# Kernel tuning notes

Measured on AMD Instinct MI355X. Metric: run time of the kernel, lower is better.

The kernel has to match this reference:

```python
import jax, jax.numpy as jnp
import numpy as np

N_NODES = 50000
N_EDGES = 1_600_000
N_GRAPHS = 64
EMB = 1280
GCN_DIMS = [128, 256, 256]
FC_DIMS = [1024, 128]
EPS = 1e-5  # BatchNorm eps (torch default)


def setup_inputs() -> dict:
    key = jax.random.key(0)
    ks = jax.random.split(key, 16)
    inp = {}
    inp["x"] = jax.random.normal(ks[0], (N_NODES, EMB), jnp.float32)
    inp["edge_index"] = jax.random.randint(ks[1], (2, N_EDGES), 0, N_NODES)
    inp["batch"] = jnp.sort(jax.random.randint(ks[2], (N_NODES,), 0, N_GRAPHS))
    dims = [EMB] + GCN_DIMS
    for i in range(3):
        inp[f"Wg{i}"] = jax.random.normal(ks[3 + i], (dims[i], dims[i + 1]), jnp.float32) * (1.0 / np.sqrt(dims[i]))
        inp[f"bg{i}"] = jnp.zeros((dims[i + 1],), jnp.float32)
        inp[f"gamma{i}"] = jnp.ones((dims[i + 1],), jnp.float32)
        inp[f"beta{i}"] = jnp.zeros((dims[i + 1],), jnp.float32)
    fdims = [GCN_DIMS[-1]] + FC_DIMS
    for i in range(2):
        inp[f"Wf{i}"] = jax.random.normal(ks[10 + i], (fdims[i], fdims[i + 1]), jnp.float32) * (1.0 / np.sqrt(fdims[i]))
        inp[f"bf{i}"] = jnp.zeros((fdims[i + 1],), jnp.float32)
    return inp


def _batchnorm(h, gamma, beta):
    # training-mode BN over node dim, biased variance (torch normalization)
    m = h.mean(axis=0)
    v = h.var(axis=0)
    return gamma * (h - m) * jax.lax.rsqrt(v + EPS) + beta


def reference(x, edge_index, batch,
              Wg0, bg0, gamma0, beta0,
              Wg1, bg1, gamma1, beta1,
              Wg2, bg2, gamma2, beta2,
              Wf0, bf0, Wf1, bf1):
    # --- GCN symmetric normalization with self-loops (PyG GCNConv default) ---
    loop = jnp.arange(N_NODES)
    src = jnp.concatenate([edge_index[0], loop])  # message sources
    dst = jnp.concatenate([edge_index[1], loop])  # aggregation targets
    deg = jax.ops.segment_sum(jnp.ones(src.shape[0], jnp.float32), dst, num_segments=N_NODES)
    dinv = jnp.where(deg > 0, jax.lax.rsqrt(jnp.maximum(deg, 1.0)), 0.0)
    norm = dinv[src] * dinv[dst]  # [E + N]

    def gcn_conv(h, W, b):
        h = h @ W                               # [N, d_out] transform first (PyG order)
        msg = h[src] * norm[:, None]            # gather + scale
        return jax.ops.segment_sum(msg, dst, num_segments=N_NODES) + b

    h = x
    for W, b, g, bt in ((Wg0, bg0, gamma0, beta0),
                        (Wg1, bg1, gamma1, beta1),
                        (Wg2, bg2, gamma2, beta2)):
        h = gcn_conv(h, W, b)
        h = _batchnorm(h, g, bt)
        h = jax.nn.relu(h)
        # dropout is identity in eval mode

    # --- global mean pool over graphs ---
    counts = jax.ops.segment_sum(jnp.ones(N_NODES, jnp.float32), batch, num_segments=N_GRAPHS)
    sums = jax.ops.segment_sum(h, batch, num_segments=N_GRAPHS)
    g = sums / jnp.maximum(counts, 1.0)[:, None]  # [B, 256]

    # --- FC head ---
    g = jax.nn.relu(g @ Wf0 + bf0)
    out = g @ Wf1 + bf1                           # [B, 128]
    return out
```

## Files before the change

kernel.cpp:

```cpp
#include <hip/hip_runtime.h>
#include <hip/hip_bf16.h>

#define N_NODES 50000
#define N_EDGES 1600000
#define N_GRAPHS 64

typedef _Float16 f16;
typedef _Float16 f16x8 __attribute__((ext_vector_type(8)));
typedef _Float16 f16x4 __attribute__((ext_vector_type(4)));
typedef _Float16 f16x2 __attribute__((ext_vector_type(2)));
typedef float f32x4 __attribute__((ext_vector_type(4)));

template <int V> struct VecT;
template <> struct VecT<2> { using type = f16x2; };
template <> struct VecT<4> { using type = f16x4; };

__global__ void init_deg(int* deg) {
    int i = blockIdx.x * blockDim.x + threadIdx.x;
    if (i < N_NODES) deg[i] = 1;
}

__global__ void deg_count(const int* __restrict__ dst, int* __restrict__ deg) {
    int e = blockIdx.x * blockDim.x + threadIdx.x;
    if (e < N_EDGES) atomicAdd(&deg[dst[e]], 1);
}

__global__ void make_dinv(const int* __restrict__ deg, float* __restrict__ dinv) {
    int i = blockIdx.x * blockDim.x + threadIdx.x;
    if (i < N_NODES) dinv[i] = rsqrtf((float)deg[i]);
}

__global__ void scan_deg(const int* __restrict__ deg, int* __restrict__ rowstart,
                         int* __restrict__ pos) {
    __shared__ int wsum[16];
    __shared__ int carry_s;
    const int t = threadIdx.x;
    const int lane = t & 63;
    const int w = t >> 6;
    if (t == 0) carry_s = 0;
    __syncthreads();
    for (int base = 0; base < N_NODES; base += 1024) {
        int i = base + t;
        int v = (i < N_NODES) ? (deg[i] - 1) : 0;
        int s = v;
#pragma unroll
        for (int off = 1; off < 64; off <<= 1) {
            int n = __shfl_up(s, off, 64);
            if (lane >= off) s += n;
        }
        if (lane == 63) wsum[w] = s;
        __syncthreads();
        if (w == 0) {
            int ws = (lane < 16) ? wsum[lane] : 0;
#pragma unroll
            for (int off = 1; off < 16; off <<= 1) {
                int n = __shfl_up(ws, off, 64);
                if (lane >= off) ws += n;
            }
            if (lane < 16) wsum[lane] = ws;
        }
        __syncthreads();
        int waveoff = (w == 0) ? 0 : wsum[w - 1];
        int carry = carry_s;
        int excl = carry + waveoff + s - v;
        if (i < N_NODES) {
            rowstart[i] = excl;
            pos[i] = excl;
        }
        __syncthreads();
        if (t == 0) carry_s = carry + wsum[15];
        __syncthreads();
    }
    if (t == 0) rowstart[N_NODES] = carry_s;
}

__global__ void csr_fill(const int* __restrict__ src, const int* __restrict__ dst,
                         const float* __restrict__ dinv, int* __restrict__ pos,
                         int2* __restrict__ csr) {
    int e = blockIdx.x * blockDim.x + threadIdx.x;
    if (e >= N_EDGES) return;
    int s = src[e], d = dst[e];
    int slot = atomicAdd(&pos[d], 1);
    csr[slot] = make_int2(s, __float_as_int(dinv[s] * dinv[d]));
}

__global__ void cast_w(const float* __restrict__ W, f16* __restrict__ Wt, int K, int N) {
    int i = blockIdx.x * blockDim.x + threadIdx.x;
    if (i >= K * N) return;
    int k = i % K, n = i / K;
    Wt[i] = (f16)W[(size_t)k * N + n];
}

__launch_bounds__(256)
__global__ void gemm_x_f16_sk(const float* __restrict__ A, const f16* __restrict__ Bt,
                              float* __restrict__ C0, float* __restrict__ C1,
                              float* __restrict__ C2, float* __restrict__ C3,
                              int M, int K) {
    const int gw = (int)((blockIdx.x * blockDim.x + threadIdx.x) >> 6);
    const int lane = threadIdx.x & 63;
    const int tile = gw >> 2, s = gw & 3;
    const int m0 = tile * 32;
    if (m0 >= M) return;
    float* __restrict__ C = (s == 0) ? C0 : (s == 1) ? C1 : (s == 2) ? C2 : C3;
    const int KC = K >> 2;
    const int kbeg = s * KC;
    const int r = lane & 15, q = lane >> 4;
    int row0 = m0 + r;       int row0c = row0 < M ? row0 : M - 1;
    int row1 = m0 + 16 + r;  int row1c = row1 < M ? row1 : M - 1;
    const float* a0 = A + (size_t)row0c * K + q * 8;
    const float* a1 = A + (size_t)row1c * K + q * 8;
    const f16* bp = Bt + (size_t)r * K + q * 8;

    f32x4 acc[2][8];
#pragma unroll
    for (int i = 0; i < 2; ++i)
#pragma unroll
        for (int j = 0; j < 8; ++j) acc[i][j] = (f32x4){0.f, 0.f, 0.f, 0.f};

    for (int k0 = kbeg; k0 < kbeg + KC; k0 += 32) {
        f16x8 af[2];
        {
            float4 u = *(const float4*)(a0 + k0);
            float4 v = *(const float4*)(a0 + k0 + 4);
            af[0] = (f16x8){(f16)u.x, (f16)u.y, (f16)u.z, (f16)u.w,
                            (f16)v.x, (f16)v.y, (f16)v.z, (f16)v.w};
            u = *(const float4*)(a1 + k0);
            v = *(const float4*)(a1 + k0 + 4);
            af[1] = (f16x8){(f16)u.x, (f16)u.y, (f16)u.z, (f16)u.w,
                            (f16)v.x, (f16)v.y, (f16)v.z, (f16)v.w};
        }
#pragma unroll
        for (int ni = 0; ni < 8; ++ni) {
            f16x8 bf = *(const f16x8*)(bp + (size_t)ni * 16 * K + k0);
            acc[0][ni] = __builtin_amdgcn_mfma_f32_16x16x32_f16(af[0], bf, acc[0][ni], 0, 0, 0);
            acc[1][ni] = __builtin_amdgcn_mfma_f32_16x16x32_f16(af[1], bf, acc[1][ni], 0, 0, 0);
        }
    }
#pragma unroll
    for (int mi = 0; mi < 2; ++mi)
#pragma unroll
        for (int j = 0; j < 4; ++j) {
            int row = m0 + mi * 16 + q * 4 + j;
            if (row < M) {
                float* cp = C + (size_t)row * 128 + r;
#pragma unroll
                for (int ni = 0; ni < 8; ++ni) cp[ni * 16] = acc[mi][ni][j];
            }
        }
}

__global__ void reduce_cast4(const float* __restrict__ c0, const float* __restrict__ c1,
                             const float* __restrict__ c2, const float* __restrict__ c3,
                             f16* __restrict__ o, int n4) {
    int i = blockIdx.x * blockDim.x + threadIdx.x;
    if (i >= n4) return;
    float4 a = ((const float4*)c0)[i];
    float4 b = ((const float4*)c1)[i];
    float4 c = ((const float4*)c2)[i];
    float4 d = ((const float4*)c3)[i];
    f16x4 r = {(f16)(a.x + b.x + c.x + d.x), (f16)(a.y + b.y + c.y + d.y),
               (f16)(a.z + b.z + c.z + d.z), (f16)(a.w + b.w + c.w + d.w)};
    ((f16x4*)o)[i] = r;
}

template <int K>
__launch_bounds__(256)
__global__ void gemm_h_f16(const f16* __restrict__ A16, const f16* __restrict__ Bt,
                           f16* __restrict__ C16, int M, int N) {
    const int wave = (int)((blockIdx.x * blockDim.x + threadIdx.x) >> 6);
    const int lane = threadIdx.x & 63;
    const int m0 = wave * 32;
    if (m0 >= M) return;
    const int col0 = blockIdx.y * 128;
    const int r = lane & 15, q = lane >> 4;
    int row0 = m0 + r;       int row0c = row0 < M ? row0 : M - 1;
    int row1 = m0 + 16 + r;  int row1c = row1 < M ? row1 : M - 1;
    const f16* a0 = A16 + (size_t)row0c * K + q * 8;
    const f16* a1 = A16 + (size_t)row1c * K + q * 8;
    const f16* bp = Bt + (size_t)(col0 + r) * K + q * 8;

    f32x4 acc[2][8];
#pragma unroll
    for (int i = 0; i < 2; ++i)
#pragma unroll
        for (int j = 0; j < 8; ++j) acc[i][j] = (f32x4){0.f, 0.f, 0.f, 0.f};

#pragma unroll
    for (int k0 = 0; k0 < K; k0 += 32) {
        f16x8 af0 = *(const f16x8*)(a0 + k0);
        f16x8 af1 = *(const f16x8*)(a1 + k0);
#pragma unroll
        for (int ni = 0; ni < 8; ++ni) {
            f16x8 bf = *(const f16x8*)(bp + (size_t)ni * 16 * K + k0);
            acc[0][ni] = __builtin_amdgcn_mfma_f32_16x16x32_f16(af0, bf, acc[0][ni], 0, 0, 0);
            acc[1][ni] = __builtin_amdgcn_mfma_f32_16x16x32_f16(af1, bf, acc[1][ni], 0, 0, 0);
        }
    }
#pragma unroll
    for (int mi = 0; mi < 2; ++mi)
#pragma unroll
        for (int j = 0; j < 4; ++j) {
            int row = m0 + mi * 16 + q * 4 + j;
            if (row < M) {
                f16* cp = C16 + (size_t)row * N + col0 + r;
#pragma unroll
                for (int ni = 0; ni < 8; ++ni) cp[ni * 16] = (f16)acc[mi][ni][j];
            }
        }
}

template <int D>
__launch_bounds__(256)
__global__ void aggregate(const f16* __restrict__ h, const int* __restrict__ rowstart,
                          const int2* __restrict__ csr, const float* __restrict__ dinv,
                          const float* __restrict__ bias, f16* __restrict__ out) {
    constexpr int V = D / 64;
    using vec = typename VecT<V>::type;
    int w = (int)((blockIdx.x * blockDim.x + threadIdx.x) >> 6);
    int lane = threadIdx.x & 63;
    if (w >= N_NODES) return;
    float acc[V];
    float di = dinv[w];
    vec self = *(const vec*)(h + (size_t)w * D + lane * V);
#pragma unroll
    for (int v = 0; v < V; ++v) acc[v] = (float)self[v] * (di * di);
    int e0 = rowstart[w], e1 = rowstart[w + 1];
    int j = e0;
    for (; j + 8 <= e1; j += 8) {
        int2 c[8];
        vec rr[8];
#pragma unroll
        for (int u = 0; u < 8; ++u) c[u] = csr[j + u];
#pragma unroll
        for (int u = 0; u < 8; ++u)
            rr[u] = *(const vec*)(h + (size_t)c[u].x * D + lane * V);
#pragma unroll
        for (int u = 0; u < 8; ++u) {
            float nm = __int_as_float(c[u].y);
#pragma unroll
            for (int v = 0; v < V; ++v) acc[v] += (float)rr[u][v] * nm;
        }
    }
    if (j + 4 <= e1) {
        int2 c0 = csr[j], c1 = csr[j + 1], c2 = csr[j + 2], c3 = csr[j + 3];
        vec r0 = *(const vec*)(h + (size_t)c0.x * D + lane * V);
        vec r1 = *(const vec*)(h + (size_t)c1.x * D + lane * V);
        vec r2 = *(const vec*)(h + (size_t)c2.x * D + lane * V);
        vec r3 = *(const vec*)(h + (size_t)c3.x * D + lane * V);
        float n0 = __int_as_float(c0.y), n1 = __int_as_float(c1.y);
        float n2 = __int_as_float(c2.y), n3 = __int_as_float(c3.y);
#pragma unroll
        for (int v = 0; v < V; ++v)
            acc[v] += (float)r0[v] * n0 + (float)r1[v] * n1 +
                      (float)r2[v] * n2 + (float)r3[v] * n3;
        j += 4;
    }
    for (; j < e1; ++j) {
        int2 c = csr[j];
        vec r = *(const vec*)(h + (size_t)c.x * D + lane * V);
        float nm = __int_as_float(c.y);
#pragma unroll
        for (int v = 0; v < V; ++v) acc[v] += (float)r[v] * nm;
    }
    vec o;
#pragma unroll
    for (int v = 0; v < V; ++v) o[v] = (f16)(acc[v] + bias[lane * V + v]);
    *(vec*)(out + (size_t)w * D + lane * V) = o;
}

template <int D>
__global__ void bn_stats(const f16* __restrict__ h, float* __restrict__ stat) {
    int f = threadIdx.x;
    int r0 = blockIdx.x * 128;
    int r1 = min(r0 + 128, N_NODES);
    float s = 0.f, s2 = 0.f;
    for (int r = r0; r < r1; ++r) {
        float v = (float)h[(size_t)r * D + f];
        s += v;
        s2 += v * v;
    }
    atomicAdd(&stat[f], s);
    atomicAdd(&stat[D + f], s2);
}

template <int D>
__global__ void bn_finalize(const float* __restrict__ stat, const float* __restrict__ gamma,
                            const float* __restrict__ beta, float* __restrict__ ss) {
    int f = threadIdx.x;
    float m = stat[f] * (1.0f / N_NODES);
    float var = stat[D + f] * (1.0f / N_NODES) - m * m;
    float sc = gamma[f] * rsqrtf(var + 1e-5f);
    ss[f] = sc;
    ss[D + f] = beta[f] - m * sc;
}

template <int D>
__global__ void bn_apply_relu(const f16* __restrict__ hin, const float* __restrict__ ss,
                              f16* __restrict__ hout) {
    int i = blockIdx.x * blockDim.x + threadIdx.x;
    if (i >= N_NODES * D / 8) return;
    int f0 = (i * 8) & (D - 1);
    f16x8 v = ((const f16x8*)hin)[i];
    f16x8 r;
#pragma unroll
    for (int j = 0; j < 8; ++j) {
        float val = (float)v[j] * ss[f0 + j] + ss[D + f0 + j];
        r[j] = (f16)(val > 0.f ? val : 0.f);
    }
    ((f16x8*)hout)[i] = r;
}

__global__ void count_batch_bs(const int* __restrict__ batch, int* __restrict__ cnt) {
    int g = threadIdx.x;
    if (g >= N_GRAPHS) return;
    int lo = 0, hi = N_NODES;
    while (lo < hi) { int mid = (lo + hi) >> 1; if (batch[mid] < g) lo = mid + 1; else hi = mid; }
    int b0 = lo;
    lo = 0; hi = N_NODES;
    while (lo < hi) { int mid = (lo + hi) >> 1; if (batch[mid] < g + 1) lo = mid + 1; else hi = mid; }
    cnt[g] = lo - b0;
}

__global__ void pool_seg(const f16* __restrict__ h, const int* __restrict__ batch,
                         float* __restrict__ psum) {
    int f = threadIdx.x;
    int r0 = blockIdx.x * 64;
    int r1 = min(r0 + 64, N_NODES);
    float acc = 0.f;
    int cur = batch[r0];
    for (int r = r0; r < r1; ++r) {
        int b = batch[r];
        if (b != cur) {
            atomicAdd(&psum[cur * 256 + f], acc);
            acc = 0.f;
            cur = b;
        }
        acc += (float)h[(size_t)r * 256 + f];
    }
    atomicAdd(&psum[cur * 256 + f], acc);
}

__global__ void pool_div(const float* __restrict__ psum, const int* __restrict__ cnt,
                         float* __restrict__ g) {
    int i = blockIdx.x * 256 + threadIdx.x;
    int b = i >> 8;
    float c = (float)max(cnt[b], 1);
    g[i] = psum[i] / c;
}

__global__ void fc_init(const float* __restrict__ b, float* __restrict__ Y, int rows, int N) {
    int i = blockIdx.x * blockDim.x + threadIdx.x;
    if (i < rows * N) Y[i] = b[i % N];
}

__global__ void fc_splitk(const float* __restrict__ X, const float* __restrict__ W,
                          float* __restrict__ Y, int K, int N, int KC) {
    int col = blockIdx.x * blockDim.x + threadIdx.x;
    int row = blockIdx.y;
    int k0 = blockIdx.z * KC;
    float acc = 0.f;
    const float* x = X + (size_t)row * K + k0;
    const float* w = W + (size_t)k0 * N + col;
#pragma unroll 8
    for (int k = 0; k < KC; ++k) acc += x[k] * w[(size_t)k * N];
    atomicAdd(&Y[(size_t)row * N + col], acc);
}

__global__ void relu_inplace(float* __restrict__ Y, int n) {
    int i = blockIdx.x * blockDim.x + threadIdx.x;
    if (i < n) Y[i] = Y[i] > 0.f ? Y[i] : 0.f;
}

extern "C" void kernel_launch(void* const* d_in, const int* in_sizes, int n_in,
                              void* d_out, int out_size, void* d_ws, size_t ws_size,
                              hipStream_t stream) {
    const float* x     = (const float*)d_in[0];
    const int*   ei    = (const int*)d_in[1];
    const int*   batch = (const int*)d_in[2];
    const float* Wg0 = (const float*)d_in[3],  *bg0 = (const float*)d_in[4];
    const float* gamma0 = (const float*)d_in[5], *beta0 = (const float*)d_in[6];
    const float* Wg1 = (const float*)d_in[7],  *bg1 = (const float*)d_in[8];
    const float* gamma1 = (const float*)d_in[9], *beta1 = (const float*)d_in[10];
    const float* Wg2 = (const float*)d_in[11], *bg2 = (const float*)d_in[12];
    const float* gamma2 = (const float*)d_in[13], *beta2 = (const float*)d_in[14];
    const float* Wf0 = (const float*)d_in[15], *bf0 = (const float*)d_in[16];
    const float* Wf1 = (const float*)d_in[17], *bf1 = (const float*)d_in[18];
    float* out = (float*)d_out;

    size_t off = 0;
    auto alloc = [&](size_t bytes) {
        void* p = (char*)d_ws + off;
        off += (bytes + 255) & ~(size_t)255;
        return p;
    };
    f16*   hA16     = (f16*)alloc((size_t)N_NODES * 256 * 2);
    float* cp32     = (float*)alloc((size_t)4 * N_NODES * 128 * 4);
    f16*   hBn16    = (f16*)cp32;
    f16*   h16      = (f16*)(cp32 + (size_t)N_NODES * 128);
    float* cp0      = cp32;
    float* cp1      = cp32 + (size_t)N_NODES * 128;
    float* cp2      = cp32 + (size_t)2 * N_NODES * 128;
    float* cp3      = cp32 + (size_t)3 * N_NODES * 128;
    int2*  csr      = (int2*)alloc((size_t)N_EDGES * 8);
    int*   deg      = (int*)alloc((size_t)N_NODES * 4);
    float* dinv     = (float*)alloc((size_t)N_NODES * 4);
    int*   rowstart = (int*)alloc((size_t)(N_NODES + 1) * 4);
    int*   pos      = (int*)alloc((size_t)N_NODES * 4);
    float* bnstat   = (float*)alloc(2 * 256 * 4);
    float* bnss     = (float*)alloc(2 * 256 * 4);
    float* psum     = (float*)alloc(64 * 256 * 4);
    int*   pcount   = (int*)alloc(64 * 4);
    float* gpool    = (float*)alloc(64 * 256 * 4);
    float* g1       = (float*)alloc(64 * 1024 * 4);
    f16*   W0t      = (f16*)alloc((size_t)1280 * 128 * 2);
    f16*   W1t      = (f16*)alloc((size_t)128 * 256 * 2);
    f16*   W2t      = (f16*)alloc((size_t)256 * 256 * 2);
    (void)ws_size;

    const int TPB = 256;
    const int nb_nodes = (N_NODES + TPB - 1) / TPB;
    const int nb_edges = (N_EDGES + TPB - 1) / TPB;

    init_deg<<<nb_nodes, TPB, 0, stream>>>(deg);
    deg_count<<<nb_edges, TPB, 0, stream>>>(ei + N_EDGES, deg);
    make_dinv<<<nb_nodes, TPB, 0, stream>>>(deg, dinv);
    scan_deg<<<1, 1024, 0, stream>>>(deg, rowstart, pos);
    csr_fill<<<nb_edges, TPB, 0, stream>>>(ei, ei + N_EDGES, dinv, pos, csr);
    cast_w<<<(1280 * 128 + 255) / 256, 256, 0, stream>>>(Wg0, W0t, 1280, 128);
    cast_w<<<(128 * 256 + 255) / 256, 256, 0, stream>>>(Wg1, W1t, 128, 256);
    cast_w<<<(256 * 256 + 255) / 256, 256, 0, stream>>>(Wg2, W2t, 256, 256);

    const int gemm_blocks = ((N_NODES + 31) / 32 * 64 + TPB - 1) / TPB;
    const int gemm_sk_blocks = ((N_NODES + 31) / 32 * 4 * 64 + TPB - 1) / TPB;
    const int agg_blocks = (N_NODES * 64 + TPB - 1) / TPB;

    gemm_x_f16_sk<<<gemm_sk_blocks, TPB, 0, stream>>>(x, W0t, cp0, cp1, cp2, cp3, N_NODES, 1280);
    reduce_cast4<<<(N_NODES * 128 / 4 + 255) / 256, 256, 0, stream>>>(cp0, cp1, cp2, cp3, hA16, N_NODES * 128 / 4);
    aggregate<128><<<agg_blocks, TPB, 0, stream>>>(hA16, rowstart, csr, dinv, bg0, hBn16);
    hipMemsetAsync(bnstat, 0, 2 * 128 * 4, stream);
    bn_stats<128><<<(N_NODES + 127) / 128, 128, 0, stream>>>(hBn16, bnstat);
    bn_finalize<128><<<1, 128, 0, stream>>>(bnstat, gamma0, beta0, bnss);
    bn_apply_relu<128><<<(N_NODES * 128 / 8 + 255) / 256, 256, 0, stream>>>(hBn16, bnss, h16);

    gemm_h_f16<128><<<dim3(gemm_blocks, 2), TPB, 0, stream>>>(h16, W1t, hA16, N_NODES, 256);
    aggregate<256><<<agg_blocks, TPB, 0, stream>>>(hA16, rowstart, csr, dinv, bg1, hBn16);
    hipMemsetAsync(bnstat, 0, 2 * 256 * 4, stream);
    bn_stats<256><<<(N_NODES + 127) / 128, 256, 0, stream>>>(hBn16, bnstat);
    bn_finalize<256><<<1, 256, 0, stream>>>(bnstat, gamma1, beta1, bnss);
    bn_apply_relu<256><<<(N_NODES * 256 / 8 + 255) / 256, 256, 0, stream>>>(hBn16, bnss, h16);

    gemm_h_f16<256><<<dim3(gemm_blocks, 2), TPB, 0, stream>>>(h16, W2t, hA16, N_NODES, 256);
    aggregate<256><<<agg_blocks, TPB, 0, stream>>>(hA16, rowstart, csr, dinv, bg2, hBn16);
    hipMemsetAsync(bnstat, 0, 2 * 256 * 4, stream);
    bn_stats<256><<<(N_NODES + 127) / 128, 256, 0, stream>>>(hBn16, bnstat);
    bn_finalize<256><<<1, 256, 0, stream>>>(bnstat, gamma2, beta2, bnss);
    bn_apply_relu<256><<<(N_NODES * 256 / 8 + 255) / 256, 256, 0, stream>>>(hBn16, bnss, h16);

    hipMemsetAsync(psum, 0, 64 * 256 * 4, stream);
    count_batch_bs<<<1, 64, 0, stream>>>(batch, pcount);
    pool_seg<<<(N_NODES + 63) / 64, 256, 0, stream>>>(h16, batch, psum);
    pool_div<<<64, 256, 0, stream>>>(psum, pcount, gpool);

    fc_init<<<(64 * 1024 + 255) / 256, 256, 0, stream>>>(bf0, g1, 64, 1024);
    fc_splitk<<<dim3(4, 64, 4), 256, 0, stream>>>(gpool, Wf0, g1, 256, 1024, 64);
    relu_inplace<<<(64 * 1024 + 255) / 256, 256, 0, stream>>>(g1, 64 * 1024);
    fc_init<<<(64 * 128 + 255) / 256, 256, 0, stream>>>(bf1, out, 64, 128);
    fc_splitk<<<dim3(1, 64, 16), 128, 0, stream>>>(g1, Wf1, out, 1024, 128, 64);
}
```

Baseline: 916.4 us.

## Pre-cast x to fp16 in tile-blocked layout and halve split-K partials

Adds a kernel that casts the input features to fp16 and rearranges them into 32-row by 32-column contiguous tiles, so the first GEMM reads small contiguous fp16 fragments instead of strided fp32 rows with in-loop conversion. The split-K factor for the first GEMM drops from 4 to 2, which halves the fp32 partial buffers and the reduction traffic. The cost is an extra full pass over x (read fp32, write fp16) plus fewer waves in flight for the GEMM.

```diff
diff --git a/kernel.cpp b/kernel.cpp
--- a/kernel.cpp
+++ b/kernel.cpp
@@ -4,6 +4,7 @@
 #define N_NODES 50000
 #define N_EDGES 1600000
 #define N_GRAPHS 64
+#define MT_TILES 1563
 
 typedef _Float16 f16;
 typedef _Float16 f16x8 __attribute__((ext_vector_type(8)));
@@ -92,24 +93,37 @@
 }
 
 __launch_bounds__(256)
-__global__ void gemm_x_f16_sk(const float* __restrict__ A, const f16* __restrict__ Bt,
-                              float* __restrict__ C0, float* __restrict__ C1,
-                              float* __restrict__ C2, float* __restrict__ C3,
-                              int M, int K) {
+__global__ void cast_x_blocked(const float* __restrict__ x, f16* __restrict__ xb) {
+    const int mt = blockIdx.x;
+    const int t = threadIdx.x;
+    const size_t base = (size_t)mt * 32 * 1280;
+    const size_t tbase = (size_t)mt * 40 * 1024;
+#pragma unroll 4
+    for (int i = 0; i < 40; ++i) {
+        int f = i * 1024 + t * 4;
+        int r = f / 1280;
+        int k = f - r * 1280;
+        float4 v = make_float4(0.f, 0.f, 0.f, 0.f);
+        if (mt * 32 + r < N_NODES) v = *(const float4*)(x + base + f);
+        int kt = k >> 5, kk = k & 31;
+        f16x4 o = {(f16)v.x, (f16)v.y, (f16)v.z, (f16)v.w};
+        *(f16x4*)(xb + tbase + (size_t)kt * 1024 + r * 32 + kk) = o;
+    }
+}
+
+__launch_bounds__(256)
+__global__ void gemm_xb_f16_sk(const f16* __restrict__ xb, const f16* __restrict__ Bt,
+                               float* __restrict__ C0, float* __restrict__ C1, int M) {
+    const int K = 1280;
     const int gw = (int)((blockIdx.x * blockDim.x + threadIdx.x) >> 6);
     const int lane = threadIdx.x & 63;
-    const int tile = gw >> 2, s = gw & 3;
-    const int m0 = tile * 32;
+    const int mt = gw >> 1, s = gw & 1;
+    const int m0 = mt * 32;
     if (m0 >= M) return;
-    float* __restrict__ C = (s == 0) ? C0 : (s == 1) ? C1 : (s == 2) ? C2 : C3;
-    const int KC = K >> 2;
-    const int kbeg = s * KC;
+    float* __restrict__ C = s ? C1 : C0;
     const int r = lane & 15, q = lane >> 4;
-    int row0 = m0 + r;       int row0c = row0 < M ? row0 : M - 1;
-    int row1 = m0 + 16 + r;  int row1c = row1 < M ? row1 : M - 1;
-    const float* a0 = A + (size_t)row0c * K + q * 8;
-    const float* a1 = A + (size_t)row1c * K + q * 8;
-    const f16* bp = Bt + (size_t)r * K + q * 8;
+    const f16* at = xb + (size_t)mt * 40 * 1024 + (size_t)s * 20 * 1024 + r * 32 + q * 8;
+    const f16* bp = Bt + (size_t)r * K + s * 640 + q * 8;
 
     f32x4 acc[2][8];
 #pragma unroll
@@ -117,23 +131,15 @@
 #pragma unroll
         for (int j = 0; j < 8; ++j) acc[i][j] = (f32x4){0.f, 0.f, 0.f, 0.f};
 
-    for (int k0 = kbeg; k0 < kbeg + KC; k0 += 32) {
-        f16x8 af[2];
-        {
-            float4 u = *(const float4*)(a0 + k0);
-            float4 v = *(const float4*)(a0 + k0 + 4);
-            af[0] = (f16x8){(f16)u.x, (f16)u.y, (f16)u.z, (f16)u.w,
-                            (f16)v.x, (f16)v.y, (f16)v.z, (f16)v.w};
-            u = *(const float4*)(a1 + k0);
-            v = *(const float4*)(a1 + k0 + 4);
-            af[1] = (f16x8){(f16)u.x, (f16)u.y, (f16)u.z, (f16)u.w,
-                            (f16)v.x, (f16)v.y, (f16)v.z, (f16)v.w};
-        }
+#pragma unroll 2
+    for (int kt = 0; kt < 20; ++kt) {
+        f16x8 a0 = *(const f16x8*)(at + kt * 1024);
+        f16x8 a1 = *(const f16x8*)(at + kt * 1024 + 512);
 #pragma unroll
         for (int ni = 0; ni < 8; ++ni) {
-            f16x8 bf = *(const f16x8*)(bp + (size_t)ni * 16 * K + k0);
-            acc[0][ni] = __builtin_amdgcn_mfma_f32_16x16x32_f16(af[0], bf, acc[0][ni], 0, 0, 0);
-            acc[1][ni] = __builtin_amdgcn_mfma_f32_16x16x32_f16(af[1], bf, acc[1][ni], 0, 0, 0);
+            f16x8 bf = *(const f16x8*)(bp + (size_t)ni * 16 * K + kt * 32);
+            acc[0][ni] = __builtin_amdgcn_mfma_f32_16x16x32_f16(a0, bf, acc[0][ni], 0, 0, 0);
+            acc[1][ni] = __builtin_amdgcn_mfma_f32_16x16x32_f16(a1, bf, acc[1][ni], 0, 0, 0);
         }
     }
 #pragma unroll
@@ -149,17 +155,13 @@
         }
 }
 
-__global__ void reduce_cast4(const float* __restrict__ c0, const float* __restrict__ c1,
-                             const float* __restrict__ c2, const float* __restrict__ c3,
-                             f16* __restrict__ o, int n4) {
+__global__ void reduce_cast(const float* __restrict__ c0, const float* __restrict__ c1,
+                            f16* __restrict__ o, int n4) {
     int i = blockIdx.x * blockDim.x + threadIdx.x;
     if (i >= n4) return;
     float4 a = ((const float4*)c0)[i];
     float4 b = ((const float4*)c1)[i];
-    float4 c = ((const float4*)c2)[i];
-    float4 d = ((const float4*)c3)[i];
-    f16x4 r = {(f16)(a.x + b.x + c.x + d.x), (f16)(a.y + b.y + c.y + d.y),
-               (f16)(a.z + b.z + c.z + d.z), (f16)(a.w + b.w + c.w + d.w)};
+    f16x4 r = {(f16)(a.x + b.x), (f16)(a.y + b.y), (f16)(a.z + b.z), (f16)(a.w + b.w)};
     ((f16x4*)o)[i] = r;
 }
 
@@ -394,13 +396,12 @@
         return p;
     };
     f16*   hA16     = (f16*)alloc((size_t)N_NODES * 256 * 2);
-    float* cp32     = (float*)alloc((size_t)4 * N_NODES * 128 * 4);
+    float* cp32     = (float*)alloc((size_t)2 * N_NODES * 128 * 4);
     f16*   hBn16    = (f16*)cp32;
     f16*   h16      = (f16*)(cp32 + (size_t)N_NODES * 128);
     float* cp0      = cp32;
     float* cp1      = cp32 + (size_t)N_NODES * 128;
-    float* cp2      = cp32 + (size_t)2 * N_NODES * 128;
-    float* cp3      = cp32 + (size_t)3 * N_NODES * 128;
+    f16*   xb       = (f16*)alloc((size_t)MT_TILES * 40 * 1024 * 2);
     int2*  csr      = (int2*)alloc((size_t)N_EDGES * 8);
     int*   deg      = (int*)alloc((size_t)N_NODES * 4);
     float* dinv     = (float*)alloc((size_t)N_NODES * 4);
@@ -421,6 +422,7 @@
     const int nb_nodes = (N_NODES + TPB - 1) / TPB;
     const int nb_edges = (N_EDGES + TPB - 1) / TPB;
 
+    cast_x_blocked<<<MT_TILES, TPB, 0, stream>>>(x, xb);
     init_deg<<<nb_nodes, TPB, 0, stream>>>(deg);
     deg_count<<<nb_edges, TPB, 0, stream>>>(ei + N_EDGES, deg);
     make_dinv<<<nb_nodes, TPB, 0, stream>>>(deg, dinv);
@@ -431,11 +433,11 @@
     cast_w<<<(256 * 256 + 255) / 256, 256, 0, stream>>>(Wg2, W2t, 256, 256);
 
     const int gemm_blocks = ((N_NODES + 31) / 32 * 64 + TPB - 1) / TPB;
-    const int gemm_sk_blocks = ((N_NODES + 31) / 32 * 4 * 64 + TPB - 1) / TPB;
+    const int gemm_sk_blocks = (MT_TILES * 2 * 64 + TPB - 1) / TPB;
     const int agg_blocks = (N_NODES * 64 + TPB - 1) / TPB;
 
-    gemm_x_f16_sk<<<gemm_sk_blocks, TPB, 0, stream>>>(x, W0t, cp0, cp1, cp2, cp3, N_NODES, 1280);
-    reduce_cast4<<<(N_NODES * 128 / 4 + 255) / 256, 256, 0, stream>>>(cp0, cp1, cp2, cp3, hA16, N_NODES * 128 / 4);
+    gemm_xb_f16_sk<<<gemm_sk_blocks, TPB, 0, stream>>>(xb, W0t, cp0, cp1, N_NODES);
+    reduce_cast<<<(N_NODES * 128 / 4 + 255) / 256, 256, 0, stream>>>(cp0, cp1, hA16, N_NODES * 128 / 4);
     aggregate<128><<<agg_blocks, TPB, 0, stream>>>(hA16, rowstart, csr, dinv, bg0, hBn16);
     hipMemsetAsync(bnstat, 0, 2 * 128 * 4, stream);
     bn_stats<128><<<(N_NODES + 127) / 128, 128, 0, stream>>>(hBn16, bnstat);
```

Measured after the change: 947.8 us. +3.4%, slower.
